# Kernel optimization log

Measured on AMD Instinct MI355X. Metric: run time of the kernel, lower is better.

## Reference

```python
import jax, jax.numpy as jnp
import numpy as np

N_E = 1024
E_DIM = 64
BETA = 0.25


def setup_inputs() -> dict:
    key = jax.random.key(0)
    k_z, k_c = jax.random.split(key)
    z = jax.random.normal(k_z, (64, E_DIM, 32, 32), dtype=jnp.float32)  # [B, e_dim, H, W]
    # Codebook initialized uniform(-1/n_e, 1/n_e) as in the torch module
    codebook = jax.random.uniform(k_c, (N_E, E_DIM), dtype=jnp.float32,
                                  minval=-1.0 / N_E, maxval=1.0 / N_E)
    return {"z": z, "codebook": codebook}


def reference(z, codebook):
    beta = BETA
    n_e, e_dim = codebook.shape
    # [B, e_dim, H, W] -> [B, H, W, e_dim]
    z_nhwc = jnp.transpose(z, (0, 2, 3, 1))
    zf = z_nhwc.reshape(-1, e_dim)  # [N, e_dim]
    # Squared Euclidean distances: ||z||^2 + ||e||^2 - 2 z.e  -> [N, n_e]
    d = (jnp.sum(zf * zf, axis=1, keepdims=True)
         + jnp.sum(codebook * codebook, axis=1)
         - 2.0 * jnp.matmul(zf, codebook.T))
    min_encoding_indices = jnp.argmin(d, axis=1)[:, None]  # [N, 1]
    min_encodings = jax.nn.one_hot(min_encoding_indices[:, 0], n_e, dtype=zf.dtype)  # [N, n_e]
    # Gather codebook rows via one-hot matmul (same math as torch version)
    z_q = jnp.matmul(min_encodings, codebook).reshape(z_nhwc.shape)  # [B,H,W,e_dim]
    sg = jax.lax.stop_gradient
    loss = (jnp.mean((sg(z_nhwc) - z_q) ** 2)
            + beta * jnp.mean((z_nhwc - sg(z_q)) ** 2))
    # Straight-through estimator
    z_q = z_nhwc + sg(z_q - z_nhwc)
    z_q = jnp.transpose(z_q, (0, 3, 1, 2))  # back to [B, e_dim, H, W]
    return (loss, z_q, min_encodings, min_encoding_indices)
```

## Files before the change

### kernel.cpp

```cpp
#include <hip/hip_runtime.h>

#define N_ROWS 65536
#define NE 1024
#define ED 64
#define ERR_GAP 8e-5f

static const size_t OFF_ZQ = 1;
static const size_t OFF_ME = 1 + 4194304;
static const size_t OFF_IDX = OFF_ME + (size_t)N_ROWS * NE;
#define ME_FLOATS ((size_t)N_ROWS * NE)
#define NBLK_ZQ 16384

#define SC_ZFRAG   0
#define SC_CBFRAG  4194304
#define SC_Z2      4259840
#define SC_PARTIAL 4325376
#define SC_FLAG    4341760

typedef __attribute__((ext_vector_type(8))) short short8v;
typedef __attribute__((ext_vector_type(4))) float f32x4;

__device__ __forceinline__ unsigned bf16_rne(float v) {
  unsigned u = __float_as_uint(v);
  return (u + 0x7FFFu + ((u >> 16) & 1u)) >> 16;
}

__device__ __forceinline__ void gld16(const void* g, void* l) {
  __builtin_amdgcn_global_load_lds(
      (const __attribute__((address_space(1))) void*)g,
      (__attribute__((address_space(3))) void*)l, 16, 0, 0);
}

__global__ __launch_bounds__(256) void k_e2cb(const float* __restrict__ cb,
                                              float* __restrict__ e2,
                                              short* __restrict__ cbfrag) {
  const int tid = blockIdx.x * 256 + threadIdx.x;
  const int ct = tid >> 6, lane = tid & 63;
  const int col = ct * 16 + (lane & 15);
  const int k0 = (lane >> 4) * 8;
  const float* __restrict__ ep = cb + (size_t)col * ED + k0;
  short* __restrict__ o = cbfrag + (size_t)ct * 2048 + lane * 8;
  #pragma unroll
  for (int ks = 0; ks < 2; ++ks) {
    short h[8], lo[8];
    #pragma unroll
    for (int i = 0; i < 8; ++i) {
      const float v = ep[ks * 32 + i];
      const unsigned hb = bf16_rne(v);
      const float res = v - __uint_as_float(hb << 16);
      h[i] = (short)hb; lo[i] = (short)bf16_rne(res);
    }
    *(short8v*)(o + (size_t)(0 * 2 + ks) * 512) = *(short8v*)h;
    *(short8v*)(o + (size_t)(1 * 2 + ks) * 512) = *(short8v*)lo;
  }
  if (threadIdx.x < 64) {
    const int j = blockIdx.x * 64 + threadIdx.x;
    const float* __restrict__ e = cb + (size_t)j * ED;
    float r[8];
    #pragma unroll
    for (int i = 0; i < 8; ++i) {
      float v = e[i]; float q = v * v;
      asm volatile("" : "+v"(q)); r[i] = q;
    }
    #pragma unroll
    for (int k = 1; k < 8; ++k)
      #pragma unroll
      for (int i = 0; i < 8; ++i) {
        float v = e[8 * k + i]; float q = v * v;
        asm volatile("" : "+v"(q)); r[i] += q;
      }
    e2[j] = ((r[0] + r[1]) + (r[2] + r[3])) + ((r[4] + r[5]) + (r[6] + r[7]));
  }
}

__global__ __launch_bounds__(256) void k_zsplit(const float* __restrict__ z,
                                                short* __restrict__ zfrag,
                                                float* __restrict__ z2) {
  __shared__ float lz[64][65];
  const int t = threadIdx.x, w = t >> 6, lane = t & 63;
  const int rt = blockIdx.x * 4 + w;
  const int rl = w * 16 + (lane & 15);
  const int n = rt * 16 + (lane & 15);
  const int b = n >> 10, hw = n & 1023;
  const float* __restrict__ zp = z + (size_t)b * 65536 + hw;
  const int k0 = (lane >> 4) * 8;
  short* __restrict__ o = zfrag + (size_t)rt * 2048 + lane * 8;
  #pragma unroll
  for (int ks = 0; ks < 2; ++ks) {
    float vv[8];
    short h[8], lo[8];
    #pragma unroll
    for (int i = 0; i < 8; ++i) {
      const float v = zp[(size_t)(ks * 32 + k0 + i) << 10];
      vv[i] = v;
      const unsigned hb = bf16_rne(v);
      const float res = v - __uint_as_float(hb << 16);
      h[i] = (short)hb; lo[i] = (short)bf16_rne(res);
    }
    #pragma unroll
    for (int i = 0; i < 8; ++i) lz[ks * 32 + k0 + i][rl] = vv[i];
    *(short8v*)(o + (size_t)(0 * 2 + ks) * 512) = *(short8v*)h;
    *(short8v*)(o + (size_t)(1 * 2 + ks) * 512) = *(short8v*)lo;
  }
  __syncthreads();
  if (t < 64) {
    float r[8];
    #pragma unroll
    for (int i = 0; i < 8; ++i) {
      const float v = lz[i][t];
      float q = v * v; asm volatile("" : "+v"(q)); r[i] = q;
    }
    #pragma unroll
    for (int k = 1; k < 8; ++k)
      #pragma unroll
      for (int i = 0; i < 8; ++i) {
        const float v = lz[8 * k + i][t];
        float q = v * v; asm volatile("" : "+v"(q)); r[i] += q;
      }
    z2[blockIdx.x * 64 + t] =
        ((r[0] + r[1]) + (r[2] + r[3])) + ((r[4] + r[5]) + (r[6] + r[7]));
  }
}

__global__ __launch_bounds__(256, 4) void k_mfma4(
    const short* __restrict__ zfrag, const short* __restrict__ cbfrag,
    const float* __restrict__ e2g, const float* __restrict__ z2g,
    float* __restrict__ idxf, int* __restrict__ flag) {
  __shared__ short lB[2][8192];
  __shared__ float e2l[1024];
  const int t = threadIdx.x, w = t >> 6, lane = t & 63;
  const int row0 = blockIdx.x * 64;

  #pragma unroll
  for (int i = 0; i < 4; ++i) {
    const int s = w * 4 + i;
    gld16(cbfrag + s * 512 + lane * 8, &lB[0][s * 512]);
  }
  gld16(e2g + w * 256 + lane * 4, &e2l[w * 256]);

  const int rtg = blockIdx.x * 4 + w;
  short8v a[2][2];
  #pragma unroll
  for (int hl = 0; hl < 2; ++hl)
    #pragma unroll
    for (int ks = 0; ks < 2; ++ks)
      a[hl][ks] = *(const short8v*)(zfrag + (size_t)(rtg * 4 + hl * 2 + ks) * 512 + lane * 8);

  float z2r[4];
  #pragma unroll
  for (int reg = 0; reg < 4; ++reg)
    z2r[reg] = z2g[row0 + w * 16 + (lane >> 4) * 4 + reg];

  float Tm[4], Ts[4]; int Tb[4];
  #pragma unroll
  for (int reg = 0; reg < 4; ++reg) { Tm[reg] = 1e30f; Ts[reg] = 1e30f; Tb[reg] = 0; }

  __syncthreads();

  int buf = 0;
  for (int c = 0; c < 16; ++c) {
    if (c < 15) {
      #pragma unroll
      for (int i = 0; i < 4; ++i) {
        const int s = w * 4 + i;
        gld16(cbfrag + (size_t)(c + 1) * 8192 + s * 512 + lane * 8,
              &lB[buf ^ 1][s * 512]);
      }
    }
    #pragma unroll 1
    for (int ctl = 0; ctl < 4; ++ctl) {
      short8v bfr[2][2];
      #pragma unroll
      for (int hl = 0; hl < 2; ++hl)
        #pragma unroll
        for (int ks = 0; ks < 2; ++ks)
          bfr[hl][ks] = *(const short8v*)&lB[buf][(ctl * 4 + hl * 2 + ks) * 512 + lane * 8];

      f32x4 acc = (f32x4)(0.0f);
      #pragma unroll
      for (int p = 0; p < 3; ++p) {
        const int pa = (p == 2) ? 1 : 0;
        const int pb = (p == 1) ? 1 : 0;
        #pragma unroll
        for (int ks = 0; ks < 2; ++ks)
          acc = __builtin_amdgcn_mfma_f32_16x16x32_bf16(a[pa][ks], bfr[pb][ks], acc, 0, 0, 0);
      }
      const int j = c * 64 + ctl * 16 + (lane & 15);
      const float e2v = e2l[j];
      #pragma unroll
      for (int reg = 0; reg < 4; ++reg) {
        const float dd = (z2r[reg] + e2v) - 2.0f * acc[reg];
        if (dd < Tm[reg]) { Ts[reg] = Tm[reg]; Tm[reg] = dd; Tb[reg] = j; }
        else { Ts[reg] = fminf(Ts[reg], dd); }
      }
    }
    __syncthreads();
    buf ^= 1;
  }

  #pragma unroll
  for (int reg = 0; reg < 4; ++reg) {
    float m = Tm[reg], s = Ts[reg]; int bi = Tb[reg];
    #pragma unroll
    for (int off = 1; off < 16; off <<= 1) {
      const float om = __shfl_xor(m, off, 64);
      const float os = __shfl_xor(s, off, 64);
      const int   oi = __shfl_xor(bi, off, 64);
      if (om < m || (om == m && oi < bi)) { s = fminf(m, os); m = om; bi = oi; }
      else { s = fminf(s, om); }
    }
    if ((lane & 15) == 0) {
      const int n = row0 + w * 16 + (lane >> 4) * 4 + reg;
      idxf[n] = (float)bi;
      flag[n] = (s - m < ERR_GAP) ? 1 : 0;
    }
  }
}

__global__ __launch_bounds__(256) void k_exact2(const float* __restrict__ z,
    const float* __restrict__ cb, const float* __restrict__ e2,
    const float* __restrict__ z2g, const int* __restrict__ flag,
    float* __restrict__ idxf) {
  __shared__ float zrow[64];
  __shared__ unsigned long long maskS;
  __shared__ float redM[4];
  __shared__ int   redI[4];
  const int t = threadIdx.x, w = t >> 6, lane = t & 63;
  const int row0 = blockIdx.x * 64;
  if (t < 64) {
    const unsigned long long mk = __ballot(flag[row0 + lane] != 0);
    if (lane == 0) maskS = mk;
  }
  __syncthreads();
  unsigned long long mask = maskS;
  while (mask) {
    const int bit = __ffsll((long long)mask) - 1; mask &= mask - 1;
    const int n = row0 + bit;
    const int b = n >> 10, hw = n & 1023;
    if (t < 64) zrow[t] = z[(size_t)b * 65536 + ((size_t)t << 10) + hw];
    __syncthreads();
    const float z2v = z2g[n];
    const float* __restrict__ e0 = cb + (size_t)t * 256;
    float a0 = 0.f, a1 = 0.f, a2 = 0.f, a3 = 0.f;
    #pragma unroll
    for (int k = 0; k < 64; ++k) {
      const float zk = zrow[k];
      a0 = fmaf(zk, e0[k],       a0);
      a1 = fmaf(zk, e0[64 + k],  a1);
      a2 = fmaf(zk, e0[128 + k], a2);
      a3 = fmaf(zk, e0[192 + k], a3);
    }
    float bm = 1e30f; int bi = 0;
    const float d0 = (z2v + e2[t * 4 + 0]) - 2.0f * a0;
    const float d1 = (z2v + e2[t * 4 + 1]) - 2.0f * a1;
    const float d2 = (z2v + e2[t * 4 + 2]) - 2.0f * a2;
    const float d3 = (z2v + e2[t * 4 + 3]) - 2.0f * a3;
    if (d0 < bm) { bm = d0; bi = t * 4 + 0; }
    if (d1 < bm) { bm = d1; bi = t * 4 + 1; }
    if (d2 < bm) { bm = d2; bi = t * 4 + 2; }
    if (d3 < bm) { bm = d3; bi = t * 4 + 3; }
    #pragma unroll
    for (int off = 1; off < 64; off <<= 1) {
      const float om = __shfl_xor(bm, off, 64);
      const int   oi = __shfl_xor(bi, off, 64);
      if (om < bm || (om == bm && oi < bi)) { bm = om; bi = oi; }
    }
    if (lane == 0) { redM[w] = bm; redI[w] = bi; }
    __syncthreads();
    if (t == 0) {
      float m = redM[0]; int i0 = redI[0];
      #pragma unroll
      for (int ww = 1; ww < 4; ++ww) {
        if (redM[ww] < m || (redM[ww] == m && redI[ww] < i0)) { m = redM[ww]; i0 = redI[ww]; }
      }
      idxf[n] = (float)i0;
    }
    __syncthreads();
  }
}

__global__ __launch_bounds__(256) void k_zq(const float* __restrict__ z,
    const float* __restrict__ cb, const float* __restrict__ idxf,
    float* __restrict__ zq, float* __restrict__ partial) {
  const int o = blockIdx.x * 256 + threadIdx.x;
  const int b = o >> 16;
  const int d = (o >> 10) & 63;
  const int hw = o & 1023;
  const int n = (b << 10) + hw;
  const int idx = (int)idxf[n];
  const float v = cb[(size_t)idx * ED + d];
  zq[o] = v;
  const float diff = z[o] - v;
  float s = diff * diff;
  #pragma unroll
  for (int off = 32; off > 0; off >>= 1) s += __shfl_xor(s, off, 64);
  __shared__ float sh[4];
  if ((threadIdx.x & 63) == 0) sh[threadIdx.x >> 6] = s;
  __syncthreads();
  if (threadIdx.x == 0)
    partial[blockIdx.x] = (sh[0] + sh[1]) + (sh[2] + sh[3]);
}

__global__ void k_loss(const float* __restrict__ partial, float* __restrict__ out0) {
  const int t = threadIdx.x;
  double s = 0.0;
  #pragma unroll
  for (int k = 0; k < NBLK_ZQ / 256; ++k) s += (double)partial[t + (k << 8)];
  #pragma unroll
  for (int off = 32; off > 0; off >>= 1) s += __shfl_xor(s, off, 64);
  __shared__ double sh[4];
  if ((t & 63) == 0) sh[t >> 6] = s;
  __syncthreads();
  if (t == 0)
    out0[0] = (float)(1.25 * ((sh[0] + sh[1]) + (sh[2] + sh[3])) / 4194304.0);
}

__global__ __launch_bounds__(256) void k_fill(float* __restrict__ me) {
  const size_t n4 = (ME_FLOATS - 3) >> 2;
  float4* __restrict__ p4 = reinterpret_cast<float4*>(me + 3);
  const size_t stride = (size_t)gridDim.x * blockDim.x;
  const float4 zero4 = make_float4(0.f, 0.f, 0.f, 0.f);
  for (size_t i = blockIdx.x * (size_t)blockDim.x + threadIdx.x; i < n4; i += stride)
    p4[i] = zero4;
  if (blockIdx.x == 0 && threadIdx.x == 0) {
    me[0] = 0.f; me[1] = 0.f; me[2] = 0.f;
    me[ME_FLOATS - 1] = 0.f;
  }
}

__global__ void k_scatter(const float* __restrict__ idxf, float* __restrict__ me) {
  const int n = blockIdx.x * 256 + threadIdx.x;
  const int idx = (int)idxf[n];
  me[(size_t)n * NE + idx] = 1.0f;
}

extern "C" void kernel_launch(void* const* d_in, const int* in_sizes, int n_in,
                              void* d_out, int out_size, void* d_ws, size_t ws_size,
                              hipStream_t stream) {
  const float* z  = (const float*)d_in[0];
  const float* cb = (const float*)d_in[1];
  float* out  = (float*)d_out;
  float* zq   = out + OFF_ZQ;
  float* me   = out + OFF_ME;
  float* idxf = out + OFF_IDX;
  float* base = me + 3;
  short* zfrag   = (short*)(base + SC_ZFRAG);
  short* cbfrag  = (short*)(base + SC_CBFRAG);
  float* z2      = base + SC_Z2;
  float* partial = base + SC_PARTIAL;
  int*   flag    = (int*)(base + SC_FLAG);
  float* e2  = (float*)((char*)d_ws + 16);

  k_e2cb<<<16, 256, 0, stream>>>(cb, e2, cbfrag);
  k_zsplit<<<1024, 256, 0, stream>>>(z, zfrag, z2);
  k_mfma4<<<1024, 256, 0, stream>>>(zfrag, cbfrag, e2, z2, idxf, flag);
  k_exact2<<<1024, 256, 0, stream>>>(z, cb, e2, z2, flag, idxf);
  k_zq<<<NBLK_ZQ, 256, 0, stream>>>(z, cb, idxf, zq, partial);
  k_loss<<<1, 256, 0, stream>>>(partial, out);
  k_fill<<<2048, 256, 0, stream>>>(me);
  k_scatter<<<N_ROWS / 256, 256, 0, stream>>>(idxf, me);
}
```

Baseline: 192.8 us.

## Fuse z split into distance kernel and one-hot scatter into z_q kernel

Merges the z transpose/bf16-split kernel into the MFMA distance kernel, so z fragments are built in registers from an LDS transpose instead of being written to and re-read from global scratch. The one-hot scatter moves into the z_q kernel, which now loops 8 times per block over a smaller grid, and the zero fill runs first. Scratch buffers move from inside the one-hot output region into the z_q region and the workspace. Together these remove two launches and the zfrag global round trip, at the cost of extra LDS work and an extra barrier in the distance kernel's prologue.

Result: slower. 198.1 us (+2.8%).

```diff
diff --git a/kernel.cpp b/kernel.cpp
--- a/kernel.cpp
+++ b/kernel.cpp
@@ -9,13 +9,10 @@
 static const size_t OFF_ME = 1 + 4194304;
 static const size_t OFF_IDX = OFF_ME + (size_t)N_ROWS * NE;
 #define ME_FLOATS ((size_t)N_ROWS * NE)
-#define NBLK_ZQ 16384
-
-#define SC_ZFRAG   0
-#define SC_CBFRAG  4194304
-#define SC_Z2      4259840
-#define SC_PARTIAL 4325376
-#define SC_FLAG    4341760
+
+#define SC_CBF  0
+#define SC_Z2   65536
+#define SC_FLAG 131072
 
 typedef __attribute__((ext_vector_type(8))) short short8v;
 typedef __attribute__((ext_vector_type(4))) float f32x4;
@@ -29,6 +26,19 @@
   __builtin_amdgcn_global_load_lds(
       (const __attribute__((address_space(1))) void*)g,
       (__attribute__((address_space(3))) void*)l, 16, 0, 0);
+}
+
+__global__ __launch_bounds__(256) void k_fill(float* __restrict__ me) {
+  const size_t n4 = (ME_FLOATS - 3) >> 2;
+  float4* __restrict__ p4 = reinterpret_cast<float4*>(me + 3);
+  const size_t stride = (size_t)gridDim.x * blockDim.x;
+  const float4 zero4 = make_float4(0.f, 0.f, 0.f, 0.f);
+  for (size_t i = blockIdx.x * (size_t)blockDim.x + threadIdx.x; i < n4; i += stride)
+    p4[i] = zero4;
+  if (blockIdx.x == 0 && threadIdx.x == 0) {
+    me[0] = 0.f; me[1] = 0.f; me[2] = 0.f;
+    me[ME_FLOATS - 1] = 0.f;
+  }
 }
 
 __global__ __launch_bounds__(256) void k_e2cb(const float* __restrict__ cb,
@@ -73,88 +83,78 @@
   }
 }
 
-__global__ __launch_bounds__(256) void k_zsplit(const float* __restrict__ z,
-                                                short* __restrict__ zfrag,
-                                                float* __restrict__ z2) {
-  __shared__ float lz[64][65];
+__global__ __launch_bounds__(256, 4) void k_dist(const float* __restrict__ z,
+    const short* __restrict__ cbfrag, const float* __restrict__ e2g,
+    float* __restrict__ z2g, float* __restrict__ idxf, int* __restrict__ flag) {
+  __shared__ float4 smem4[2320];
+  short* lBs = (short*)smem4;
+  float* e2l = (float*)(smem4 + 2048);
+  float* z2l = (float*)(smem4 + 2304);
+  float (*lzf)[65] = (float(*)[65])smem4;
+
   const int t = threadIdx.x, w = t >> 6, lane = t & 63;
-  const int rt = blockIdx.x * 4 + w;
+  const int row0 = blockIdx.x * 64;
+
+  gld16(e2g + w * 256 + lane * 4, e2l + w * 256);
+
   const int rl = w * 16 + (lane & 15);
-  const int n = rt * 16 + (lane & 15);
-  const int b = n >> 10, hw = n & 1023;
-  const float* __restrict__ zp = z + (size_t)b * 65536 + hw;
+  const int n0 = row0 + rl;
+  const int bb = n0 >> 10, hw = n0 & 1023;
+  const float* __restrict__ zp = z + (size_t)bb * 65536 + hw;
   const int k0 = (lane >> 4) * 8;
-  short* __restrict__ o = zfrag + (size_t)rt * 2048 + lane * 8;
+  #pragma unroll
+  for (int ks = 0; ks < 2; ++ks)
+    #pragma unroll
+    for (int i = 0; i < 8; ++i)
+      lzf[ks * 32 + k0 + i][rl] = zp[(size_t)(ks * 32 + k0 + i) << 10];
+  __syncthreads();
+
+  short8v a[2][2];
   #pragma unroll
   for (int ks = 0; ks < 2; ++ks) {
-    float vv[8];
     short h[8], lo[8];
     #pragma unroll
     for (int i = 0; i < 8; ++i) {
-      const float v = zp[(size_t)(ks * 32 + k0 + i) << 10];
-      vv[i] = v;
+      const float v = lzf[ks * 32 + k0 + i][rl];
       const unsigned hb = bf16_rne(v);
       const float res = v - __uint_as_float(hb << 16);
       h[i] = (short)hb; lo[i] = (short)bf16_rne(res);
     }
-    #pragma unroll
-    for (int i = 0; i < 8; ++i) lz[ks * 32 + k0 + i][rl] = vv[i];
-    *(short8v*)(o + (size_t)(0 * 2 + ks) * 512) = *(short8v*)h;
-    *(short8v*)(o + (size_t)(1 * 2 + ks) * 512) = *(short8v*)lo;
-  }
-  __syncthreads();
+    a[0][ks] = *(short8v*)h;
+    a[1][ks] = *(short8v*)lo;
+  }
   if (t < 64) {
     float r[8];
     #pragma unroll
     for (int i = 0; i < 8; ++i) {
-      const float v = lz[i][t];
+      const float v = lzf[i][t];
       float q = v * v; asm volatile("" : "+v"(q)); r[i] = q;
     }
     #pragma unroll
     for (int k = 1; k < 8; ++k)
       #pragma unroll
       for (int i = 0; i < 8; ++i) {
-        const float v = lz[8 * k + i][t];
+        const float v = lzf[8 * k + i][t];
         float q = v * v; asm volatile("" : "+v"(q)); r[i] += q;
       }
-    z2[blockIdx.x * 64 + t] =
-        ((r[0] + r[1]) + (r[2] + r[3])) + ((r[4] + r[5]) + (r[6] + r[7]));
-  }
-}
-
-__global__ __launch_bounds__(256, 4) void k_mfma4(
-    const short* __restrict__ zfrag, const short* __restrict__ cbfrag,
-    const float* __restrict__ e2g, const float* __restrict__ z2g,
-    float* __restrict__ idxf, int* __restrict__ flag) {
-  __shared__ short lB[2][8192];
-  __shared__ float e2l[1024];
-  const int t = threadIdx.x, w = t >> 6, lane = t & 63;
-  const int row0 = blockIdx.x * 64;
+    const float z2v = ((r[0] + r[1]) + (r[2] + r[3])) + ((r[4] + r[5]) + (r[6] + r[7]));
+    z2g[row0 + t] = z2v;
+    z2l[t] = z2v;
+  }
+  __syncthreads();
 
   #pragma unroll
   for (int i = 0; i < 4; ++i) {
     const int s = w * 4 + i;
-    gld16(cbfrag + s * 512 + lane * 8, &lB[0][s * 512]);
-  }
-  gld16(e2g + w * 256 + lane * 4, &e2l[w * 256]);
-
-  const int rtg = blockIdx.x * 4 + w;
-  short8v a[2][2];
-  #pragma unroll
-  for (int hl = 0; hl < 2; ++hl)
-    #pragma unroll
-    for (int ks = 0; ks < 2; ++ks)
-      a[hl][ks] = *(const short8v*)(zfrag + (size_t)(rtg * 4 + hl * 2 + ks) * 512 + lane * 8);
-
+    gld16(cbfrag + s * 512 + lane * 8, lBs + s * 512);
+  }
   float z2r[4];
   #pragma unroll
   for (int reg = 0; reg < 4; ++reg)
-    z2r[reg] = z2g[row0 + w * 16 + (lane >> 4) * 4 + reg];
-
+    z2r[reg] = z2l[w * 16 + (lane >> 4) * 4 + reg];
   float Tm[4], Ts[4]; int Tb[4];
   #pragma unroll
   for (int reg = 0; reg < 4; ++reg) { Tm[reg] = 1e30f; Ts[reg] = 1e30f; Tb[reg] = 0; }
-
   __syncthreads();
 
   int buf = 0;
@@ -164,7 +164,7 @@
       for (int i = 0; i < 4; ++i) {
         const int s = w * 4 + i;
         gld16(cbfrag + (size_t)(c + 1) * 8192 + s * 512 + lane * 8,
-              &lB[buf ^ 1][s * 512]);
+              lBs + (buf ^ 1) * 8192 + s * 512);
       }
     }
     #pragma unroll 1
@@ -174,7 +174,8 @@
       for (int hl = 0; hl < 2; ++hl)
         #pragma unroll
         for (int ks = 0; ks < 2; ++ks)
-          bfr[hl][ks] = *(const short8v*)&lB[buf][(ctl * 4 + hl * 2 + ks) * 512 + lane * 8];
+          bfr[hl][ks] = *(const short8v*)(lBs + buf * 8192 +
+              (ctl * 4 + hl * 2 + ks) * 512 + lane * 8);
 
       f32x4 acc = (f32x4)(0.0f);
       #pragma unroll
@@ -281,17 +282,22 @@
 
 __global__ __launch_bounds__(256) void k_zq(const float* __restrict__ z,
     const float* __restrict__ cb, const float* __restrict__ idxf,
-    float* __restrict__ zq, float* __restrict__ partial) {
-  const int o = blockIdx.x * 256 + threadIdx.x;
-  const int b = o >> 16;
-  const int d = (o >> 10) & 63;
-  const int hw = o & 1023;
-  const int n = (b << 10) + hw;
-  const int idx = (int)idxf[n];
-  const float v = cb[(size_t)idx * ED + d];
-  zq[o] = v;
-  const float diff = z[o] - v;
-  float s = diff * diff;
+    float* __restrict__ zq, float* __restrict__ partial, float* __restrict__ me) {
+  float s = 0.f;
+  #pragma unroll 1
+  for (int it = 0; it < 8; ++it) {
+    const int o = (it * 2048 + blockIdx.x) * 256 + threadIdx.x;
+    const int b = o >> 16;
+    const int d = (o >> 10) & 63;
+    const int hw = o & 1023;
+    const int n = (b << 10) + hw;
+    const int idx = (int)idxf[n];
+    const float v = cb[(size_t)idx * ED + d];
+    zq[o] = v;
+    if (d == 0) me[(size_t)n * NE + idx] = 1.0f;
+    const float diff = z[o] - v;
+    s = fmaf(diff, diff, s);
+  }
   #pragma unroll
   for (int off = 32; off > 0; off >>= 1) s += __shfl_xor(s, off, 64);
   __shared__ float sh[4];
@@ -305,7 +311,7 @@
   const int t = threadIdx.x;
   double s = 0.0;
   #pragma unroll
-  for (int k = 0; k < NBLK_ZQ / 256; ++k) s += (double)partial[t + (k << 8)];
+  for (int k = 0; k < 8; ++k) s += (double)partial[t + (k << 8)];
   #pragma unroll
   for (int off = 32; off > 0; off >>= 1) s += __shfl_xor(s, off, 64);
   __shared__ double sh[4];
@@ -313,25 +319,6 @@
   __syncthreads();
   if (t == 0)
     out0[0] = (float)(1.25 * ((sh[0] + sh[1]) + (sh[2] + sh[3])) / 4194304.0);
-}
-
-__global__ __launch_bounds__(256) void k_fill(float* __restrict__ me) {
-  const size_t n4 = (ME_FLOATS - 3) >> 2;
-  float4* __restrict__ p4 = reinterpret_cast<float4*>(me + 3);
-  const size_t stride = (size_t)gridDim.x * blockDim.x;
-  const float4 zero4 = make_float4(0.f, 0.f, 0.f, 0.f);
-  for (size_t i = blockIdx.x * (size_t)blockDim.x + threadIdx.x; i < n4; i += stride)
-    p4[i] = zero4;
-  if (blockIdx.x == 0 && threadIdx.x == 0) {
-    me[0] = 0.f; me[1] = 0.f; me[2] = 0.f;
-    me[ME_FLOATS - 1] = 0.f;
-  }
-}
-
-__global__ void k_scatter(const float* __restrict__ idxf, float* __restrict__ me) {
-  const int n = blockIdx.x * 256 + threadIdx.x;
-  const int idx = (int)idxf[n];
-  me[(size_t)n * NE + idx] = 1.0f;
 }
 
 extern "C" void kernel_launch(void* const* d_in, const int* in_sizes, int n_in,
@@ -343,20 +330,17 @@
   float* zq   = out + OFF_ZQ;
   float* me   = out + OFF_ME;
   float* idxf = out + OFF_IDX;
-  float* base = me + 3;
-  short* zfrag   = (short*)(base + SC_ZFRAG);
-  short* cbfrag  = (short*)(base + SC_CBFRAG);
-  float* z2      = base + SC_Z2;
-  float* partial = base + SC_PARTIAL;
-  int*   flag    = (int*)(base + SC_FLAG);
-  float* e2  = (float*)((char*)d_ws + 16);
-
+  float* sbase = out + 4;
+  short* cbfrag = (short*)(sbase + SC_CBF);
+  float* z2     = sbase + SC_Z2;
+  int*   flag   = (int*)(sbase + SC_FLAG);
+  float* e2      = (float*)((char*)d_ws + 16);
+  float* partial = (float*)((char*)d_ws + 4112);
+
+  k_fill<<<2048, 256, 0, stream>>>(me);
   k_e2cb<<<16, 256, 0, stream>>>(cb, e2, cbfrag);
-  k_zsplit<<<1024, 256, 0, stream>>>(z, zfrag, z2);
-  k_mfma4<<<1024, 256, 0, stream>>>(zfrag, cbfrag, e2, z2, idxf, flag);
+  k_dist<<<1024, 256, 0, stream>>>(z, cbfrag, e2, z2, idxf, flag);
   k_exact2<<<1024, 256, 0, stream>>>(z, cb, e2, z2, flag, idxf);
-  k_zq<<<NBLK_ZQ, 256, 0, stream>>>(z, cb, idxf, zq, partial);
+  k_zq<<<2048, 256, 0, stream>>>(z, cb, idxf, zq, partial, me);
   k_loss<<<1, 256, 0, stream>>>(partial, out);
-  k_fill<<<2048, 256, 0, stream>>>(me);
-  k_scatter<<<N_ROWS / 256, 256, 0, stream>>>(idxf, me);
-}
+}
```
